# Performance work log

Measured on AMD Instinct MI355X. Metric: run time of the kernel, lower is better.

The kernel has to match this reference:

```python
import jax, jax.numpy as jnp
import numpy as np

WORD_EMB_DIM = 100
TAG_EMB_DIM = 28
EMB_DIM = WORD_EMB_DIM + TAG_EMB_DIM  # 128; LSTM hidden size per direction
HID = EMB_DIM
WORD_VOCAB = 50000
TAG_VOCAB = 50
B = 16
L = 128


def _lstm_dir(x, w_ih, w_hh, b_ih, b_hh, reverse):
    # x: [B, T, In] -> [B, T, H]; PyTorch gate order i, f, g, o
    xT = jnp.swapaxes(x, 0, 1)  # [T, B, In]
    if reverse:
        xT = xT[::-1]
    xp = jnp.einsum('tbi,gi->tbg', xT, w_ih) + b_ih + b_hh  # [T, B, 4H]
    H = w_hh.shape[1]

    def step(carry, g_x):
        h, c = carry
        g = g_x + h @ w_hh.T
        i, f, gg, o = jnp.split(g, 4, axis=-1)
        c = jax.nn.sigmoid(f) * c + jax.nn.sigmoid(i) * jnp.tanh(gg)
        h = jax.nn.sigmoid(o) * jnp.tanh(c)
        return (h, c), h

    h0 = jnp.zeros((x.shape[0], H), x.dtype)
    _, hs = jax.lax.scan(step, (h0, h0), xp)
    if reverse:
        hs = hs[::-1]
    return jnp.swapaxes(hs, 0, 1)


def _bilstm(x, pf, pb):
    return jnp.concatenate([_lstm_dir(x, *pf, reverse=False),
                            _lstm_dir(x, *pb, reverse=True)], axis=-1)


def setup_inputs() -> dict:
    key = jax.random.key(0)
    ks = iter(jax.random.split(key, 40))

    def rn(shape, s=0.1):
        return (jax.random.normal(next(ks), shape) * s).astype(jnp.float32)

    inp = {
        'words_idx': jax.random.randint(next(ks), (B, L), 0, WORD_VOCAB),
        'pos_idx': jax.random.randint(next(ks), (B, L), 0, TAG_VOCAB),
        'max_length': L,
        'lengths': jax.random.randint(next(ks), (B,), 1, L + 1),
        'word_emb': rn((WORD_VOCAB, WORD_EMB_DIM)),
        'tag_emb': rn((TAG_VOCAB, TAG_EMB_DIM)),
    }
    for l, insz in ((0, EMB_DIM), (1, 2 * HID)):
        for d in ('f', 'b'):
            inp[f'w_ih_l{l}{d}'] = rn((4 * HID, insz))
            inp[f'w_hh_l{l}{d}'] = rn((4 * HID, HID))
            inp[f'b_ih_l{l}{d}'] = rn((4 * HID,))
            inp[f'b_hh_l{l}{d}'] = rn((4 * HID,))
    inp['fc1_w'] = rn((100, 4 * EMB_DIM))
    inp['fc1_b'] = rn((100,))
    inp['fc2_w'] = rn((1, 100))
    inp['fc2_b'] = rn((1,))
    return inp


def reference(words_idx, pos_idx, max_length, lengths, word_emb, tag_emb,
              w_ih_l0f, w_hh_l0f, b_ih_l0f, b_hh_l0f,
              w_ih_l0b, w_hh_l0b, b_ih_l0b, b_hh_l0b,
              w_ih_l1f, w_hh_l1f, b_ih_l1f, b_hh_l1f,
              w_ih_l1b, w_hh_l1b, b_ih_l1b, b_hh_l1b,
              fc1_w, fc1_b, fc2_w, fc2_b):
    # embeddings + concat -> [B, L, EMB_DIM]
    x = jnp.concatenate([word_emb[words_idx[:, :max_length]],
                         tag_emb[pos_idx[:, :max_length]]], axis=-1)
    h = _bilstm(x, (w_ih_l0f, w_hh_l0f, b_ih_l0f, b_hh_l0f),
                (w_ih_l0b, w_hh_l0b, b_ih_l0b, b_hh_l0b))
    h = _bilstm(h, (w_ih_l1f, w_hh_l1f, b_ih_l1f, b_hh_l1f),
                (w_ih_l1b, w_hh_l1b, b_ih_l1b, b_hh_l1b))  # [B, L, 2*HID]
    # Pairwise feature(i,j) = cat(h[:,i], h[:,j]); fuse fc1 by splitting its
    # weight into head/dependent halves -> broadcast-add instead of L^2 concat.
    D = h.shape[-1]
    wa, wb = fc1_w[:, :D], fc1_w[:, D:]
    a = jnp.einsum('bld,kd->blk', h, wa)                 # [B, L, 100]
    bp = jnp.einsum('bld,kd->blk', h, wb) + fc1_b        # [B, L, 100]
    hid = jnp.tanh(a[:, :, None, :] + bp[:, None, :, :])  # [B, L, L, 100]
    scores = jnp.einsum('bijk,ok->bijo', hid, fc2_w) + fc2_b  # [B, L, L, 1]
    # original stacks features along axis 0 in (i outer, j inner) order
    return scores.transpose(1, 2, 0, 3).reshape(max_length * max_length, -1, 1)
```

## Files before the change

### kernel.cpp

```cpp
#include <hip/hip_runtime.h>

typedef float v2f __attribute__((ext_vector_type(2)));

__device__ __forceinline__ float frcp(float x){ return __builtin_amdgcn_rcpf(x); }
__device__ __forceinline__ float fexp2(float x){ return __builtin_amdgcn_exp2f(x); }
__device__ __forceinline__ float sigf(float x){ return frcp(1.f + fexp2(-1.4426950408889634f*x)); }
__device__ __forceinline__ float tanh_(float x){ return 1.f - 2.f*frcp(1.f + fexp2(2.8853900817779268f*x)); }

__global__ __launch_bounds__(256) void embed_kernel(
    const int* __restrict__ widx, const int* __restrict__ pidx,
    const float* __restrict__ wemb, const float* __restrict__ temb,
    float* __restrict__ x)
{
    int gid = blockIdx.x*256 + threadIdx.x;
    int bt = gid >> 7, c = gid & 127;
    float v;
    if (c < 100) v = wemb[(size_t)widx[bt]*100 + c];
    else         v = temb[(size_t)pidx[bt]*28 + (c-100)];
    x[gid] = v;
}

__global__ __launch_bounds__(256) void gemm_kernel(
    const float* __restrict__ A, int K,
    const float* __restrict__ B0, const float* __restrict__ B1, int ldb,
    const float* __restrict__ bias0a, const float* __restrict__ bias0b,
    const float* __restrict__ bias1a, const float* __restrict__ bias1b,
    float* __restrict__ C0, float* __restrict__ C1, int ldc, int N,
    int expflag, int permflag)
{
    __shared__ float As[16][140];
    __shared__ float Bs[16][68];
    const int z = blockIdx.z;
    const float* B  = z ? B1 : B0;
    const float* ba = z ? bias1a : bias0a;
    const float* bb = z ? bias1b : bias0b;
    float* C = z ? C1 : C0;
    const int m0 = blockIdx.x * 128;
    const int n0 = blockIdx.y * 64;
    const int tx = threadIdx.x;
    const int tm = tx & 15, tn = tx >> 4;
    const int arow = tx >> 1, akq = (tx & 1) * 8;
    const int brow = tx >> 2, bkq = (tx & 3) * 4;
    const int g_arow = arow + 4*(arow >> 5);
    const int rbase = tm*8 + 4*(tm >> 2);
    float acc[8][4];
    #pragma unroll
    for (int r=0;r<8;++r){
        #pragma unroll
        for (int c=0;c<4;++c) acc[r][c]=0.f; }
    const int bn = n0 + brow;
    const int brow_src = permflag ? ((bn & 3)*128 + (bn >> 2)) : bn;
    for (int k0 = 0; k0 < K; k0 += 16) {
        const float* ap = A + (size_t)(m0+arow)*K + k0 + akq;
        float4 a0 = *(const float4*)ap;
        float4 a1 = *(const float4*)(ap+4);
        float4 bv = make_float4(0.f,0.f,0.f,0.f);
        if (bn < N) {
            const float* bp = B + (size_t)brow_src*ldb + k0 + bkq;
            bv = *(const float4*)bp;
        }
        __syncthreads();
        As[akq+0][g_arow]=a0.x; As[akq+1][g_arow]=a0.y; As[akq+2][g_arow]=a0.z; As[akq+3][g_arow]=a0.w;
        As[akq+4][g_arow]=a1.x; As[akq+5][g_arow]=a1.y; As[akq+6][g_arow]=a1.z; As[akq+7][g_arow]=a1.w;
        Bs[bkq+0][brow]=bv.x; Bs[bkq+1][brow]=bv.y; Bs[bkq+2][brow]=bv.z; Bs[bkq+3][brow]=bv.w;
        __syncthreads();
        #pragma unroll
        for (int kk = 0; kk < 16; ++kk) {
            float4 av0 = *(const float4*)&As[kk][rbase];
            float4 av1 = *(const float4*)&As[kk][rbase+4];
            float4 bvv = *(const float4*)&Bs[kk][tn*4];
            float a[8] = {av0.x,av0.y,av0.z,av0.w,av1.x,av1.y,av1.z,av1.w};
            float b[4] = {bvv.x,bvv.y,bvv.z,bvv.w};
            #pragma unroll
            for (int r=0;r<8;++r){
                #pragma unroll
                for (int c=0;c<4;++c)
                    acc[r][c] = fmaf(a[r], b[c], acc[r][c]);
            }
        }
    }
    float bias[4];
    #pragma unroll
    for (int c=0;c<4;++c) {
        int n = n0 + tn*4 + c;
        int nsrc = permflag ? ((n & 3)*128 + (n >> 2)) : n;
        float v = 0.f;
        if (n < N) {
            if (ba) v += ba[nsrc];
            if (bb) v += bb[nsrc];
        }
        bias[c] = v;
    }
    #pragma unroll
    for (int r=0;r<8;++r) {
        int m = m0 + tm*8 + r;
        float v[4];
        #pragma unroll
        for (int c=0;c<4;++c) {
            float t = acc[r][c] + bias[c];
            if (expflag) t = fexp2(fminf(fmaxf(t,-40.f),40.f)*2.8853900817779268f);
            v[c] = t;
        }
        int n = n0 + tn*4;
        if (n + 3 < N) {
            float4 st; st.x=v[0]; st.y=v[1]; st.z=v[2]; st.w=v[3];
            *(float4*)&C[(size_t)m*ldc + n] = st;
        } else {
            #pragma unroll
            for (int c=0;c<4;++c) if (n+c < N) C[(size_t)m*ldc + n + c] = v[c];
        }
    }
}

__global__ __launch_bounds__(512, 2)
void lstm_kernel(
    const float* __restrict__ xp,
    const float* __restrict__ whh_f, const float* __restrict__ whh_b,
    float* __restrict__ hcat)
{
    const int b = blockIdx.x & 15;
    const int dir = blockIdx.x >> 4;
    const int t = threadIdx.x;
    const int half = t & 1;
    const int p = t >> 1;
    const int gate = p & 3, rp = p >> 2;
    const int lane = t & 63, gbase = lane & ~7;
    const float* whh = dir ? whh_b : whh_f;
    const float kexp = (gate == 2) ? 2.8853900817779268f : -1.4426950408889634f;
    const float mA   = (gate == 2) ? -2.f : 1.f;
    const float mB   = (gate == 2) ?  1.f : 0.f;

    v2f w[64];
    {
        const float* wr = whh + (size_t)(gate*128 + 2*rp)*128 + 64*half;
        #pragma unroll
        for (int j = 0; j < 64; j += 4) {
            float4 a = *(const float4*)(wr + j);
            float4 bq = *(const float4*)(wr + 128 + j);
            w[j+0] = (v2f){a.x, bq.x};
            w[j+1] = (v2f){a.y, bq.y};
            w[j+2] = (v2f){a.z, bq.z};
            w[j+3] = (v2f){a.w, bq.w};
        }
    }

    __shared__ float h_lds[2][136];
    float c = 0.f;
    if (t < 128) h_lds[0][t + 4*(t >> 6)] = 0.f;
    __syncthreads();
    const float* xpd = xp + (size_t)dir*(2048*512) + (size_t)b*(128*512);
    const int myrow = 2*rp + half;
    const int mycol = 4*myrow + gate;
    const int mystore = myrow + 4*(myrow >> 6);
    float xpv = xpd[(dir ? 127 : 0)*512 + mycol];
    const int koff = 68*half;
    for (int s = 0; s < 128; ++s) {
        #pragma unroll
        for (int j = 0; j < 64; ++j) asm volatile("" : "+v"(w[j]));
        const int ts = dir ? (127 - s) : s;
        const int tsn = dir ? (126 - s < 0 ? 0 : 126 - s) : (s + 1 > 127 ? 127 : s + 1);
        float xnext = xpd[tsn*512 + mycol];
        const float* hb = &h_lds[s & 1][koff];
        v2f da = (v2f){0.f,0.f}, db = (v2f){0.f,0.f};
        #pragma unroll
        for (int j = 0; j < 64; j += 4) {
            float4 h4 = *(const float4*)&hb[j];
            da += w[j+0] * (v2f){h4.x, h4.x};
            db += w[j+1] * (v2f){h4.y, h4.y};
            da += w[j+2] * (v2f){h4.z, h4.z};
            db += w[j+3] * (v2f){h4.w, h4.w};
        }
        v2f d = da + db;
        float d0 = d.x + __shfl_xor(d.x, 1, 64);
        float d1 = d.y + __shfl_xor(d.y, 1, 64);
        float dot = xpv + (half ? d1 : d0);
        float act = fmaf(mA, frcp(1.f + fexp2(kexp*dot)), mB);
        float i_ = __shfl(act, gbase + 0 + half, 64);
        float f_ = __shfl(act, gbase + 2 + half, 64);
        float g_ = __shfl(act, gbase + 4 + half, 64);
        float o_ = __shfl(act, gbase + 6 + half, 64);
        c = f_*c + i_*g_;
        float h = o_ * tanh_(c);
        if ((lane & 7) < 2) {
            h_lds[(s & 1) ^ 1][mystore] = h;
            hcat[((size_t)b*128 + ts)*256 + dir*128 + myrow] = h;
        }
        xpv = xnext;
        __syncthreads();
    }
}

__global__ __launch_bounds__(256) void pair_kernel(
    const float* __restrict__ ea, const float* __restrict__ eb,
    const float* __restrict__ fc2w, const float* __restrict__ fc2b,
    float* __restrict__ out)
{
    __shared__ float eas[32][100];
    __shared__ float ebs[32][100];
    __shared__ float w2s[100];
    __shared__ float red[128];
    const int it = blockIdx.x * 32, jt = blockIdx.y * 32, b = blockIdx.z;
    const int tx = threadIdx.x;
    const float* eab = ea + (size_t)b*12800;
    const float* ebb = eb + (size_t)b*12800;
    for (int idx = tx; idx < 3200; idx += 256) {
        int r = idx / 100;
        int cc = idx - r*100;
        eas[r][cc] = eab[(it + r)*100 + cc];
        ebs[r][cc] = ebb[(jt + r)*100 + cc];
    }
    if (tx < 128) {
        float wv = (tx < 100) ? fc2w[tx] : 0.f;
        if (tx < 100) w2s[tx] = -2.f*wv;
        red[tx] = wv;
    }
    __syncthreads();
    for (int s2 = 64; s2 > 0; s2 >>= 1) {
        if (tx < s2) red[tx] += red[tx+s2];
        __syncthreads();
    }
    const float S = red[0] + fc2b[0];
    const int jp = tx & 15, ip = tx >> 4;
    const int i0 = ip*2, j0 = jp*2;
    float acc00=S, acc01=S, acc10=S, acc11=S;
    #pragma unroll
    for (int k = 0; k < 100; k += 4) {
        float4 A0 = *(const float4*)&eas[i0][k];
        float4 A1 = *(const float4*)&eas[i0+1][k];
        float4 B0 = *(const float4*)&ebs[j0][k];
        float4 B1 = *(const float4*)&ebs[j0+1][k];
        float4 W  = *(const float4*)&w2s[k];
        acc00 = fmaf(W.x, frcp(fmaf(A0.x,B0.x,1.f)), acc00);
        acc01 = fmaf(W.x, frcp(fmaf(A0.x,B1.x,1.f)), acc01);
        acc10 = fmaf(W.x, frcp(fmaf(A1.x,B0.x,1.f)), acc10);
        acc11 = fmaf(W.x, frcp(fmaf(A1.x,B1.x,1.f)), acc11);
        acc00 = fmaf(W.y, frcp(fmaf(A0.y,B0.y,1.f)), acc00);
        acc01 = fmaf(W.y, frcp(fmaf(A0.y,B1.y,1.f)), acc01);
        acc10 = fmaf(W.y, frcp(fmaf(A1.y,B0.y,1.f)), acc10);
        acc11 = fmaf(W.y, frcp(fmaf(A1.y,B1.y,1.f)), acc11);
        acc00 = fmaf(W.z, frcp(fmaf(A0.z,B0.z,1.f)), acc00);
        acc01 = fmaf(W.z, frcp(fmaf(A0.z,B1.z,1.f)), acc01);
        acc10 = fmaf(W.z, frcp(fmaf(A1.z,B0.z,1.f)), acc10);
        acc11 = fmaf(W.z, frcp(fmaf(A1.z,B1.z,1.f)), acc11);
        acc00 = fmaf(W.w, frcp(fmaf(A0.w,B0.w,1.f)), acc00);
        acc01 = fmaf(W.w, frcp(fmaf(A0.w,B1.w,1.f)), acc01);
        acc10 = fmaf(W.w, frcp(fmaf(A1.w,B0.w,1.f)), acc10);
        acc11 = fmaf(W.w, frcp(fmaf(A1.w,B1.w,1.f)), acc11);
    }
    const int gi0 = it + i0, gj0 = jt + j0;
    out[((size_t)(gi0  )*128 + gj0  )*16 + b] = acc00;
    out[((size_t)(gi0  )*128 + gj0+1)*16 + b] = acc01;
    out[((size_t)(gi0+1)*128 + gj0  )*16 + b] = acc10;
    out[((size_t)(gi0+1)*128 + gj0+1)*16 + b] = acc11;
}

extern "C" void kernel_launch(void* const* d_in, const int* in_sizes, int n_in,
                              void* d_out, int out_size, void* d_ws, size_t ws_size,
                              hipStream_t stream)
{
    (void)in_sizes; (void)n_in; (void)out_size; (void)ws_size;
    const int*   widx = (const int*)d_in[0];
    const int*   pidx = (const int*)d_in[1];
    const float* wemb = (const float*)d_in[4];
    const float* temb = (const float*)d_in[5];
    const float* w_ih_l0f = (const float*)d_in[6];
    const float* w_hh_l0f = (const float*)d_in[7];
    const float* b_ih_l0f = (const float*)d_in[8];
    const float* b_hh_l0f = (const float*)d_in[9];
    const float* w_ih_l0b = (const float*)d_in[10];
    const float* w_hh_l0b = (const float*)d_in[11];
    const float* b_ih_l0b = (const float*)d_in[12];
    const float* b_hh_l0b = (const float*)d_in[13];
    const float* w_ih_l1f = (const float*)d_in[14];
    const float* w_hh_l1f = (const float*)d_in[15];
    const float* b_ih_l1f = (const float*)d_in[16];
    const float* b_hh_l1f = (const float*)d_in[17];
    const float* w_ih_l1b = (const float*)d_in[18];
    const float* w_hh_l1b = (const float*)d_in[19];
    const float* b_ih_l1b = (const float*)d_in[20];
    const float* b_hh_l1b = (const float*)d_in[21];
    const float* fc1_w = (const float*)d_in[22];
    const float* fc1_b = (const float*)d_in[23];
    const float* fc2_w = (const float*)d_in[24];
    const float* fc2_b = (const float*)d_in[25];

    float* ws  = (float*)d_ws;
    float* x   = ws;
    float* xp0 = x + 262144;
    float* h1  = xp0 + 2097152;
    float* xp1 = h1 + 524288;
    float* h2  = xp1 + 2097152;
    float* ea  = h2 + 524288;
    float* eb  = ea + 204800;

    embed_kernel<<<1024, 256, 0, stream>>>(widx, pidx, wemb, temb, x);
    gemm_kernel<<<dim3(16,8,2), 256, 0, stream>>>(x, 128,
        w_ih_l0f, w_ih_l0b, 128,
        b_ih_l0f, b_hh_l0f, b_ih_l0b, b_hh_l0b,
        xp0, xp0 + 1048576, 512, 512, 0, 1);
    lstm_kernel<<<32, 512, 0, stream>>>(xp0, w_hh_l0f, w_hh_l0b, h1);
    gemm_kernel<<<dim3(16,8,2), 256, 0, stream>>>(h1, 256,
        w_ih_l1f, w_ih_l1b, 256,
        b_ih_l1f, b_hh_l1f, b_ih_l1b, b_hh_l1b,
        xp1, xp1 + 1048576, 512, 512, 0, 1);
    lstm_kernel<<<32, 512, 0, stream>>>(xp1, w_hh_l1f, w_hh_l1b, h2);
    gemm_kernel<<<dim3(16,2,2), 256, 0, stream>>>(h2, 256,
        fc1_w, fc1_w + 256, 512,
        nullptr, nullptr, fc1_b, nullptr,
        ea, eb, 100, 100, 1, 0);
    pair_kernel<<<dim3(4,4,16), 256, 0, stream>>>(ea, eb, fc2_w, fc2_b, (float*)d_out);
}
```

Measured before the change: 396.6 us.

## Restructure LSTM recurrence: 4-way K split, 4 rows per thread, swizzle gate combine

Each thread in the LSTM kernel now holds weights for 4 hidden rows of one gate over a quarter of K, instead of 2 rows over half of K. Partial dot products are reduced with a two-stage xor shuffle. Gate combination replaces four indexed shuffles with two ds_swizzle exchanges and select logic. The aim is to shorten the per-step serial dependency chain and the cross-lane exchange cost in the recurrence. It also drops the asm register pins and the restrict qualifiers, which may change register allocation or cause spills.

```diff
diff --git a/kernel.cpp b/kernel.cpp
--- a/kernel.cpp
+++ b/kernel.cpp
@@ -115,73 +115,80 @@
 __global__ __launch_bounds__(512, 2)
 void lstm_kernel(
     const float* __restrict__ xp,
-    const float* __restrict__ whh_f, const float* __restrict__ whh_b,
-    float* __restrict__ hcat)
+    const float* whh_f, const float* whh_b,
+    float* hcat)
 {
     const int b = blockIdx.x & 15;
     const int dir = blockIdx.x >> 4;
     const int t = threadIdx.x;
-    const int half = t & 1;
-    const int p = t >> 1;
-    const int gate = p & 3, rp = p >> 2;
-    const int lane = t & 63, gbase = lane & ~7;
+    const int q  = t & 3;
+    const int gc = (t >> 2) & 3;
+    const int rp = t >> 4;
     const float* whh = dir ? whh_b : whh_f;
-    const float kexp = (gate == 2) ? 2.8853900817779268f : -1.4426950408889634f;
-    const float mA   = (gate == 2) ? -2.f : 1.f;
-    const float mB   = (gate == 2) ?  1.f : 0.f;
-
-    v2f w[64];
+    const int G = (gc == 0) ? 0 : (gc == 1) ? 2 : (gc == 2) ? 1 : 3;
+    const float kexp = (gc == 1) ? 2.8853900817779268f : -1.4426950408889634f;
+    const float mA   = (gc == 1) ? -2.f : 1.f;
+    const float mB   = (gc == 1) ?  1.f : 0.f;
+
+    v2f wA[32], wB[32];
     {
-        const float* wr = whh + (size_t)(gate*128 + 2*rp)*128 + 64*half;
-        #pragma unroll
-        for (int j = 0; j < 64; j += 4) {
-            float4 a = *(const float4*)(wr + j);
-            float4 bq = *(const float4*)(wr + 128 + j);
-            w[j+0] = (v2f){a.x, bq.x};
-            w[j+1] = (v2f){a.y, bq.y};
-            w[j+2] = (v2f){a.z, bq.z};
-            w[j+3] = (v2f){a.w, bq.w};
-        }
-    }
-
-    __shared__ float h_lds[2][136];
+        const float* wr = whh + (size_t)(G*128 + 4*rp)*128 + 32*q;
+        #pragma unroll
+        for (int j = 0; j < 32; j += 4) {
+            float4 r0 = *(const float4*)(wr + j);
+            float4 r1 = *(const float4*)(wr + 128 + j);
+            float4 r2 = *(const float4*)(wr + 256 + j);
+            float4 r3 = *(const float4*)(wr + 384 + j);
+            wA[j+0] = (v2f){r0.x, r1.x}; wB[j+0] = (v2f){r2.x, r3.x};
+            wA[j+1] = (v2f){r0.y, r1.y}; wB[j+1] = (v2f){r2.y, r3.y};
+            wA[j+2] = (v2f){r0.z, r1.z}; wB[j+2] = (v2f){r2.z, r3.z};
+            wA[j+3] = (v2f){r0.w, r1.w}; wB[j+3] = (v2f){r2.w, r3.w};
+        }
+    }
+
+    __shared__ float h_lds[2][140];
     float c = 0.f;
-    if (t < 128) h_lds[0][t + 4*(t >> 6)] = 0.f;
+    if (t < 128) h_lds[0][t + 4*(t >> 5)] = 0.f;
     __syncthreads();
+
     const float* xpd = xp + (size_t)dir*(2048*512) + (size_t)b*(128*512);
-    const int myrow = 2*rp + half;
-    const int mycol = 4*myrow + gate;
-    const int mystore = myrow + 4*(myrow >> 6);
+    const int myrow = 4*rp + q;
+    const int mycol = 4*myrow + G;
+    const int mystore = myrow + 4*(myrow >> 5);
     float xpv = xpd[(dir ? 127 : 0)*512 + mycol];
-    const int koff = 68*half;
+
     for (int s = 0; s < 128; ++s) {
-        #pragma unroll
-        for (int j = 0; j < 64; ++j) asm volatile("" : "+v"(w[j]));
         const int ts = dir ? (127 - s) : s;
         const int tsn = dir ? (126 - s < 0 ? 0 : 126 - s) : (s + 1 > 127 ? 127 : s + 1);
         float xnext = xpd[tsn*512 + mycol];
-        const float* hb = &h_lds[s & 1][koff];
-        v2f da = (v2f){0.f,0.f}, db = (v2f){0.f,0.f};
-        #pragma unroll
-        for (int j = 0; j < 64; j += 4) {
+        const float* hb = &h_lds[s & 1][36*q];
+        v2f aA = (v2f){0.f,0.f}, aB = (v2f){0.f,0.f};
+        #pragma unroll
+        for (int j = 0; j < 32; j += 4) {
             float4 h4 = *(const float4*)&hb[j];
-            da += w[j+0] * (v2f){h4.x, h4.x};
-            db += w[j+1] * (v2f){h4.y, h4.y};
-            da += w[j+2] * (v2f){h4.z, h4.z};
-            db += w[j+3] * (v2f){h4.w, h4.w};
-        }
-        v2f d = da + db;
-        float d0 = d.x + __shfl_xor(d.x, 1, 64);
-        float d1 = d.y + __shfl_xor(d.y, 1, 64);
-        float dot = xpv + (half ? d1 : d0);
+            aA += wA[j+0] * (v2f){h4.x, h4.x};  aB += wB[j+0] * (v2f){h4.x, h4.x};
+            aA += wA[j+1] * (v2f){h4.y, h4.y};  aB += wB[j+1] * (v2f){h4.y, h4.y};
+            aA += wA[j+2] * (v2f){h4.z, h4.z};  aB += wB[j+2] * (v2f){h4.z, h4.z};
+            aA += wA[j+3] * (v2f){h4.w, h4.w};  aB += wB[j+3] * (v2f){h4.w, h4.w};
+        }
+        float a0 = aA.x, a1 = aA.y, a2 = aB.x, a3 = aB.y;
+        a0 += __shfl_xor(a0, 1, 64); a1 += __shfl_xor(a1, 1, 64);
+        a2 += __shfl_xor(a2, 1, 64); a3 += __shfl_xor(a3, 1, 64);
+        a0 += __shfl_xor(a0, 2, 64); a1 += __shfl_xor(a1, 2, 64);
+        a2 += __shfl_xor(a2, 2, 64); a3 += __shfl_xor(a3, 2, 64);
+        float dsel = (q & 2) ? ((q & 1) ? a3 : a2) : ((q & 1) ? a1 : a0);
+        float dot = xpv + dsel;
         float act = fmaf(mA, frcp(1.f + fexp2(kexp*dot)), mB);
-        float i_ = __shfl(act, gbase + 0 + half, 64);
-        float f_ = __shfl(act, gbase + 2 + half, 64);
-        float g_ = __shfl(act, gbase + 4 + half, 64);
-        float o_ = __shfl(act, gbase + 6 + half, 64);
-        c = f_*c + i_*g_;
-        float h = o_ * tanh_(c);
-        if ((lane & 7) < 2) {
+        float o1 = __uint_as_float(__builtin_amdgcn_ds_swizzle(__float_as_uint(act), 0x101F));
+        float v1 = (gc < 2) ? act * o1 : ((gc == 2) ? act : o1);
+        float o2 = __uint_as_float(__builtin_amdgcn_ds_swizzle(__float_as_uint(v1), 0x201F));
+        float Af = (gc < 2) ? o2 : ((gc == 2) ? act : o1);
+        float Bf = (gc < 2) ? v1 : o2;
+        c = fmaf(Af, c, Bf);
+        float th = tanh_(c);
+        float sigo = (gc == 2) ? o1 : act;
+        float h = sigo * th;
+        if (gc == 2) {
             h_lds[(s & 1) ^ 1][mystore] = h;
             hcat[((size_t)b*128 + ts)*256 + dir*128 + myrow] = h;
         }
```

Result: no change. 392.9 us (-1.0%).

## Pack LSTM recurrent weights to fp16 and use fdot2 with one gate-row per thread

Applied to the files above, without the earlier changes.

Adds a pack kernel that converts each direction's recurrent weight matrix to packed fp16 pairs, laid out per thread. The LSTM step now gives each thread a full 128-wide gate row, held as 64 half2 registers. It computes the dot product with fdot2 against an fp16 copy of h kept in LDS. This removes the half-row split and its cross-lane shuffle reduction and halves the LDS traffic for h. The cost is reduced precision in the recurrent matmul and hidden state, plus two extra small kernel launches per call.

```diff
diff --git a/kernel.cpp b/kernel.cpp
--- a/kernel.cpp
+++ b/kernel.cpp
@@ -1,11 +1,17 @@
 #include <hip/hip_runtime.h>
 
 typedef float v2f __attribute__((ext_vector_type(2)));
+typedef _Float16 h2 __attribute__((ext_vector_type(2)));
 
 __device__ __forceinline__ float frcp(float x){ return __builtin_amdgcn_rcpf(x); }
 __device__ __forceinline__ float fexp2(float x){ return __builtin_amdgcn_exp2f(x); }
-__device__ __forceinline__ float sigf(float x){ return frcp(1.f + fexp2(-1.4426950408889634f*x)); }
 __device__ __forceinline__ float tanh_(float x){ return 1.f - 2.f*frcp(1.f + fexp2(2.8853900817779268f*x)); }
+
+#if __has_builtin(__builtin_amdgcn_fdot2)
+#define FDOT2(a,b,c) __builtin_amdgcn_fdot2((a),(b),(c),false)
+#else
+#define FDOT2(a,b,c) ((c) + (float)(a).x*(float)(b).x + (float)(a).y*(float)(b).y)
+#endif
 
 __global__ __launch_bounds__(256) void embed_kernel(
     const int* __restrict__ widx, const int* __restrict__ pidx,
@@ -18,6 +24,20 @@
     if (c < 100) v = wemb[(size_t)widx[bt]*100 + c];
     else         v = temb[(size_t)pidx[bt]*28 + (c-100)];
     x[gid] = v;
+}
+
+__global__ __launch_bounds__(256) void pack_kernel(
+    const float* __restrict__ whh_f, const float* __restrict__ whh_b,
+    unsigned* __restrict__ wpack)
+{
+    int id = blockIdx.x*256 + threadIdx.x;
+    int d = id >> 15, t = (id >> 6) & 511, j = id & 63;
+    const float* whh = d ? whh_b : whh_f;
+    int r = t >> 2, g = t & 3;
+    const float* src = whh + (size_t)(g*128 + r)*128 + 2*j;
+    unsigned short a = __builtin_bit_cast(unsigned short, (_Float16)src[0]);
+    unsigned short b = __builtin_bit_cast(unsigned short, (_Float16)src[1]);
+    wpack[((size_t)d*512 + t)*64 + j] = (unsigned)a | ((unsigned)b << 16);
 }
 
 __global__ __launch_bounds__(256) void gemm_kernel(
@@ -115,75 +135,63 @@
 __global__ __launch_bounds__(512, 2)
 void lstm_kernel(
     const float* __restrict__ xp,
-    const float* __restrict__ whh_f, const float* __restrict__ whh_b,
-    float* __restrict__ hcat)
+    const unsigned* wpk,
+    float* hcat)
 {
     const int b = blockIdx.x & 15;
     const int dir = blockIdx.x >> 4;
     const int t = threadIdx.x;
-    const int half = t & 1;
-    const int p = t >> 1;
-    const int gate = p & 3, rp = p >> 2;
-    const int lane = t & 63, gbase = lane & ~7;
-    const float* whh = dir ? whh_b : whh_f;
+    const int gate = t & 3, r = t >> 2;
+    const int lane = t & 63, qbase = lane & ~3;
     const float kexp = (gate == 2) ? 2.8853900817779268f : -1.4426950408889634f;
     const float mA   = (gate == 2) ? -2.f : 1.f;
     const float mB   = (gate == 2) ?  1.f : 0.f;
 
-    v2f w[64];
+    h2 w[64];
     {
-        const float* wr = whh + (size_t)(gate*128 + 2*rp)*128 + 64*half;
+        const unsigned* wr = wpk + ((size_t)dir*512 + t)*64;
         #pragma unroll
         for (int j = 0; j < 64; j += 4) {
-            float4 a = *(const float4*)(wr + j);
-            float4 bq = *(const float4*)(wr + 128 + j);
-            w[j+0] = (v2f){a.x, bq.x};
-            w[j+1] = (v2f){a.y, bq.y};
-            w[j+2] = (v2f){a.z, bq.z};
-            w[j+3] = (v2f){a.w, bq.w};
-        }
-    }
-
-    __shared__ float h_lds[2][136];
+            uint4 u = *(const uint4*)(wr + j);
+            w[j+0] = __builtin_bit_cast(h2, u.x);
+            w[j+1] = __builtin_bit_cast(h2, u.y);
+            w[j+2] = __builtin_bit_cast(h2, u.z);
+            w[j+3] = __builtin_bit_cast(h2, u.w);
+        }
+    }
+
+    __shared__ _Float16 h_lds[2][128];
     float c = 0.f;
-    if (t < 128) h_lds[0][t + 4*(t >> 6)] = 0.f;
+    if (t < 128) h_lds[0][t] = (_Float16)0.f;
     __syncthreads();
+
     const float* xpd = xp + (size_t)dir*(2048*512) + (size_t)b*(128*512);
-    const int myrow = 2*rp + half;
-    const int mycol = 4*myrow + gate;
-    const int mystore = myrow + 4*(myrow >> 6);
-    float xpv = xpd[(dir ? 127 : 0)*512 + mycol];
-    const int koff = 68*half;
+    float xpv = xpd[(dir ? 127 : 0)*512 + t];
     for (int s = 0; s < 128; ++s) {
-        #pragma unroll
-        for (int j = 0; j < 64; ++j) asm volatile("" : "+v"(w[j]));
         const int ts = dir ? (127 - s) : s;
         const int tsn = dir ? (126 - s < 0 ? 0 : 126 - s) : (s + 1 > 127 ? 127 : s + 1);
-        float xnext = xpd[tsn*512 + mycol];
-        const float* hb = &h_lds[s & 1][koff];
-        v2f da = (v2f){0.f,0.f}, db = (v2f){0.f,0.f};
-        #pragma unroll
-        for (int j = 0; j < 64; j += 4) {
-            float4 h4 = *(const float4*)&hb[j];
-            da += w[j+0] * (v2f){h4.x, h4.x};
-            db += w[j+1] * (v2f){h4.y, h4.y};
-            da += w[j+2] * (v2f){h4.z, h4.z};
-            db += w[j+3] * (v2f){h4.w, h4.w};
-        }
-        v2f d = da + db;
-        float d0 = d.x + __shfl_xor(d.x, 1, 64);
-        float d1 = d.y + __shfl_xor(d.y, 1, 64);
-        float dot = xpv + (half ? d1 : d0);
+        float xnext = xpd[tsn*512 + t];
+        const uint4* hb = (const uint4*)&h_lds[s & 1][0];
+        float A0=0.f, A1=0.f, A2=0.f, A3=0.f;
+        #pragma unroll
+        for (int j = 0; j < 16; ++j) {
+            uint4 u = hb[j];
+            A0 = FDOT2(w[4*j+0], __builtin_bit_cast(h2, u.x), A0);
+            A1 = FDOT2(w[4*j+1], __builtin_bit_cast(h2, u.y), A1);
+            A2 = FDOT2(w[4*j+2], __builtin_bit_cast(h2, u.z), A2);
+            A3 = FDOT2(w[4*j+3], __builtin_bit_cast(h2, u.w), A3);
+        }
+        float dot = xpv + ((A0+A1)+(A2+A3));
         float act = fmaf(mA, frcp(1.f + fexp2(kexp*dot)), mB);
-        float i_ = __shfl(act, gbase + 0 + half, 64);
-        float f_ = __shfl(act, gbase + 2 + half, 64);
-        float g_ = __shfl(act, gbase + 4 + half, 64);
-        float o_ = __shfl(act, gbase + 6 + half, 64);
+        float i_ = __shfl(act, qbase+0, 64);
+        float f_ = __shfl(act, qbase+1, 64);
+        float g_ = __shfl(act, qbase+2, 64);
+        float o_ = __shfl(act, qbase+3, 64);
         c = f_*c + i_*g_;
         float h = o_ * tanh_(c);
-        if ((lane & 7) < 2) {
-            h_lds[(s & 1) ^ 1][mystore] = h;
-            hcat[((size_t)b*128 + ts)*256 + dir*128 + myrow] = h;
+        if (gate == 0) {
+            h_lds[(s & 1) ^ 1][r] = (_Float16)h;
+            hcat[((size_t)b*128 + ts)*256 + dir*128 + r] = h;
         }
         xpv = xnext;
         __syncthreads();
@@ -292,18 +300,22 @@
     float* h2  = xp1 + 2097152;
     float* ea  = h2 + 524288;
     float* eb  = ea + 204800;
+    unsigned* wpk0 = (unsigned*)(eb + 204800);
+    unsigned* wpk1 = wpk0 + 65536;
 
     embed_kernel<<<1024, 256, 0, stream>>>(widx, pidx, wemb, temb, x);
+    pack_kernel<<<256, 256, 0, stream>>>(w_hh_l0f, w_hh_l0b, wpk0);
+    pack_kernel<<<256, 256, 0, stream>>>(w_hh_l1f, w_hh_l1b, wpk1);
     gemm_kernel<<<dim3(16,8,2), 256, 0, stream>>>(x, 128,
         w_ih_l0f, w_ih_l0b, 128,
         b_ih_l0f, b_hh_l0f, b_ih_l0b, b_hh_l0b,
         xp0, xp0 + 1048576, 512, 512, 0, 1);
-    lstm_kernel<<<32, 512, 0, stream>>>(xp0, w_hh_l0f, w_hh_l0b, h1);
+    lstm_kernel<<<32, 512, 0, stream>>>(xp0, wpk0, h1);
     gemm_kernel<<<dim3(16,8,2), 256, 0, stream>>>(h1, 256,
         w_ih_l1f, w_ih_l1b, 256,
         b_ih_l1f, b_hh_l1f, b_ih_l1b, b_hh_l1b,
         xp1, xp1 + 1048576, 512, 512, 0, 1);
-    lstm_kernel<<<32, 512, 0, stream>>>(xp1, w_hh_l1f, w_hh_l1b, h2);
+    lstm_kernel<<<32, 512, 0, stream>>>(xp1, wpk1, h2);
     gemm_kernel<<<dim3(16,2,2), 256, 0, stream>>>(h2, 256,
         fc1_w, fc1_w + 256, 512,
         nullptr, nullptr, fc1_b, nullptr,
```

Measured after the change: 359.4 us. 1.1x faster.
